# Optimization experiments

Measured on AMD Instinct MI355X. Metric: run time of the kernel, lower is better.

## Reference

```python
import jax, jax.numpy as jnp
import numpy as np

NUM_HEADS = 16
HEAD_DIM = 64
G_CONST = 1.0        # phase='fluid'
CURVATURE = 0.15     # phase='fluid'
EPS = 1e-06


def setup_inputs() -> dict:
    key = jax.random.key(0)
    k1, k2, k3, k4, k5 = jax.random.split(key, 5)
    B, S, D = 4, 4096, 1024
    x = jax.random.normal(k1, (B, S, D), dtype=jnp.float32)
    W_qkv = jax.random.normal(k2, (D, 3 * D), dtype=jnp.float32) * 0.02
    b_qkv = jax.random.normal(k3, (3 * D,), dtype=jnp.float32) * 0.02
    W_out = jax.random.normal(k4, (D, D), dtype=jnp.float32) * 0.02
    b_out = jax.random.normal(k5, (D,), dtype=jnp.float32) * 0.02
    return {"x": x, "W_qkv": W_qkv, "b_qkv": b_qkv, "W_out": W_out, "b_out": b_out}


def reference(x, W_qkv, b_qkv, W_out, b_out):
    B, S, D = x.shape
    H, Hd = NUM_HEADS, HEAD_DIM
    # qkv projection -> (B, S, 3, H, Hd); heads are NOT transposed (faithful to source):
    # attention is computed among the H heads at each token position.
    qkv = (x @ W_qkv + b_qkv).reshape(B, S, 3, H, Hd)
    q, k, v = qkv[:, :, 0], qkv[:, :, 1], qkv[:, :, 2]  # each (B,S,H,Hd)

    # squared euclidean distances between head vectors (matmul-based cdist, clamped >= 0)
    q_sq = jnp.sum(q * q, axis=-1)                      # (B,S,H)
    k_sq = jnp.sum(k * k, axis=-1)                      # (B,S,H)
    qk = jnp.einsum('bshd,bsgd->bshg', q, k)            # (B,S,H,H)
    dist_sq = jnp.maximum(q_sq[..., :, None] + k_sq[..., None, :] - 2.0 * qk, 0.0)

    # curvature cosine modulation (curvature != 0 in 'fluid' phase)
    dist_sq = dist_sq * (1.0 + CURVATURE * jnp.cos(jnp.sqrt(dist_sq + EPS)))

    # gravitational forces: G * m_q m_k / (d^2 + eps)
    m_q = jnp.sqrt(q_sq)                                # (B,S,H)
    m_k = jnp.sqrt(k_sq)                                # (B,S,H)
    forces = G_CONST * (m_q[..., :, None] * m_k[..., None, :]) / (dist_sq + EPS)

    attn = jax.nn.softmax(forces, axis=-1)              # softmax over key-heads
    out = jnp.einsum('bshg,bsgd->bshd', attn, v).reshape(B, S, D)
    return out @ W_out + b_out
```

## Files before the change

kernel.cpp:

```cpp
#include <hip/hip_runtime.h>
#include <hip/hip_bf16.h>
#include <math.h>

#define M_TOTAL 16384
#define D_MODEL 1024
#define N_QKV   3072
#define CURV    0.15f
#define EPS_F   1e-6f

typedef __attribute__((ext_vector_type(8))) short short8v;
typedef __attribute__((ext_vector_type(4))) float f32x4;

__device__ __forceinline__ void gl_lds16(const void* g, void* l) {
    __builtin_amdgcn_global_load_lds(
        (const __attribute__((address_space(1))) void*)g,
        (__attribute__((address_space(3))) void*)l, 16, 0, 0);
}
__device__ __forceinline__ unsigned short f2bf_bits(float x) {
    __hip_bfloat16 t = __float2bfloat16(x);
    return *(unsigned short*)&t;
}
__device__ __forceinline__ float bf2f(unsigned short u) {
    return __uint_as_float(((unsigned)u) << 16);
}

__global__ __launch_bounds__(256)
void cast_f32_bf16(const float* __restrict__ in, unsigned short* __restrict__ out,
                   int ngroups)
{
    int i = blockIdx.x * 256 + threadIdx.x;
    if (i >= ngroups) return;
    float4 u = ((const float4*)in)[i];
    ushort4 r;
    r.x = f2bf_bits(u.x); r.y = f2bf_bits(u.y);
    r.z = f2bf_bits(u.z); r.w = f2bf_bits(u.w);
    ((ushort4*)out)[i] = r;
}

__global__ __launch_bounds__(256)
void transpose_cast(const float* __restrict__ W, unsigned short* __restrict__ Wt,
                    int K, int N)
{
    __shared__ float tile[32][33];
    const int n0 = blockIdx.x * 32;
    const int k0 = blockIdx.y * 32;
    const int tx = threadIdx.x & 31;
    const int ty = threadIdx.x >> 5;
    #pragma unroll
    for (int i = 0; i < 32; i += 8)
        tile[ty + i][tx] = W[(size_t)(k0 + ty + i) * N + n0 + tx];
    __syncthreads();
    #pragma unroll
    for (int i = 0; i < 32; i += 8)
        Wt[(size_t)(n0 + ty + i) * K + k0 + tx] = f2bf_bits(tile[tx][ty + i]);
}

template<int OUT_BF16>
__global__ __launch_bounds__(512, 2)
void gemm256_8ph(const unsigned short* __restrict__ A,
                 const unsigned short* __restrict__ Bt,
                 const float* __restrict__ bias,
                 void* __restrict__ Cout,
                 int M, int N, int K, int nbx)
{
    __shared__ __align__(16) short smem_s[65536];

    const int t    = threadIdx.x;
    const int w    = t >> 6;
    const int lane = t & 63;
    const int wm   = w >> 2;
    const int wn   = w & 3;
    const int lr   = lane & 15;
    const int hi   = lane >> 4;
    const int lo7  = lane & 7;

    const int nwg  = gridDim.x;
    const int orig = blockIdx.x;
    const int wgid = (orig & 7) * (nwg >> 3) + (orig >> 3);
    const int by = wgid / nbx, bx = wgid % nbx;
    const int bm0 = by * 256, bn0 = bx * 256;

    const int nt = K >> 6;

    const int srow = t >> 3;
    const int scol = ((t & 7) ^ (srow & 7)) * 8;
    const unsigned short* Ag = A  + (size_t)(bm0 + srow) * K + scol;
    const unsigned short* Bg = Bt + (size_t)(bn0 + srow) * K + scol;
    const int wbase = w * 1024;

    auto STAGE = [&](int which, int half, int tile) {
        const unsigned short* g0 = (which ? Bg : Ag)
                                 + (size_t)(half * 128) * K + (size_t)tile * 64;
        char* d0 = (char*)smem_s + ((tile & 1) * 65536 + which * 32768
                                    + half * 16384 + wbase);
        gl_lds16(g0,                d0);
        gl_lds16(g0 + (size_t)64*K, d0 + 8192);
    };

    short8v a[8][2], b[4][2];
    f32x4 acc[8][4] = {};

    auto LDA = [&](int buf, int m, int ks) {
        a[m][ks] = *(const short8v*)&smem_s[buf*32768 + wm*8192
                        + (m*16 + lr)*64 + (((ks*4 + hi) ^ lo7) * 8)];
    };
    auto LDB = [&](int buf, int n, int ks) {
        b[n][ks] = *(const short8v*)&smem_s[buf*32768 + 16384 + (wn>>1)*8192
                        + ((wn&1)*64 + n*16 + lr)*64 + (((ks*4 + hi) ^ lo7) * 8)];
    };
    auto QUAD = [&](int mlo, int nlo) {
        __builtin_amdgcn_s_setprio(1);
        #pragma unroll
        for (int mi = 0; mi < 4; ++mi)
            #pragma unroll
            for (int ni = 0; ni < 2; ++ni)
                #pragma unroll
                for (int ks = 0; ks < 2; ++ks)
                    acc[mlo+mi][nlo+ni] = __builtin_amdgcn_mfma_f32_16x16x32_bf16(
                        a[mlo+mi][ks], b[nlo+ni][ks], acc[mlo+mi][nlo+ni], 0, 0, 0);
        __builtin_amdgcn_s_setprio(0);
    };

    STAGE(0,0,0); STAGE(0,1,0); STAGE(1,0,0); STAGE(1,1,0);
    STAGE(0,0,1); STAGE(0,1,1); STAGE(1,0,1); STAGE(1,1,1);
    asm volatile("s_waitcnt vmcnt(8)" ::: "memory");
    __builtin_amdgcn_s_barrier();
    #pragma unroll
    for (int m = 0; m < 4; ++m) { LDA(0,m,0); LDA(0,m,1); }
    LDB(0,0,0); LDB(0,0,1); LDB(0,1,0); LDB(0,1,1);

    for (int T = 0; T < nt; ++T) {
        const int buf  = T & 1;
        const int nbuf = buf ^ 1;
        LDB(buf,2,0); LDB(buf,2,1); LDB(buf,3,0); LDB(buf,3,1);
        asm volatile("s_waitcnt lgkmcnt(4)" ::: "memory");
        __builtin_amdgcn_sched_barrier(0);
        QUAD(0,0);
        #pragma unroll
        for (int m = 4; m < 8; ++m) { LDA(buf,m,0); LDA(buf,m,1); }
        asm volatile("s_waitcnt lgkmcnt(8)" ::: "memory");
        __builtin_amdgcn_sched_barrier(0);
        QUAD(0,2);
        __builtin_amdgcn_s_barrier();
        if (T+2 < nt) { STAGE(1,0,T+2); STAGE(1,1,T+2); }
        asm volatile("s_waitcnt lgkmcnt(0)" ::: "memory");
        __builtin_amdgcn_sched_barrier(0);
        QUAD(4,0);
        __builtin_amdgcn_s_barrier();
        if (T+2 < nt) { STAGE(0,0,T+2); STAGE(0,1,T+2); }
        if (T+2 < nt) { asm volatile("s_waitcnt vmcnt(8)" ::: "memory"); }
        else          { asm volatile("s_waitcnt vmcnt(0)" ::: "memory"); }
        __builtin_amdgcn_s_barrier();
        if (T+1 < nt) {
            #pragma unroll
            for (int m = 0; m < 4; ++m) { LDA(nbuf,m,0); LDA(nbuf,m,1); }
            LDB(nbuf,0,0); LDB(nbuf,0,1); LDB(nbuf,1,0); LDB(nbuf,1,1);
        }
        __builtin_amdgcn_sched_barrier(0);
        QUAD(4,2);
    }

    const int r0 = bm0 + wm*128 + hi*4;
    const int cb = bn0 + wn*64 + lr;
    float bv[4];
    #pragma unroll
    for (int n = 0; n < 4; ++n) bv[n] = bias[cb + n*16];
    if (OUT_BF16) {
        unsigned short* Cb = (unsigned short*)Cout;
        #pragma unroll
        for (int m = 0; m < 8; ++m)
            #pragma unroll
            for (int j = 0; j < 4; ++j) {
                unsigned short* rp = Cb + (size_t)(r0 + m*16 + j) * N;
                #pragma unroll
                for (int n = 0; n < 4; ++n)
                    rp[cb + n*16] = f2bf_bits(acc[m][n][j] + bv[n]);
            }
    } else {
        float* Cf = (float*)Cout;
        #pragma unroll
        for (int m = 0; m < 8; ++m)
            #pragma unroll
            for (int j = 0; j < 4; ++j) {
                float* rp = Cf + (size_t)(r0 + m*16 + j) * N;
                #pragma unroll
                for (int n = 0; n < 4; ++n)
                    rp[cb + n*16] = acc[m][n][j] + bv[n];
            }
    }
}

__global__ __launch_bounds__(256)
void attn_mfma_kernel(const unsigned short* __restrict__ qkv,
                      unsigned short* __restrict__ aout)
{
    const int l  = threadIdx.x & 63;
    const int wv = threadIdx.x >> 6;
    const int p  = blockIdx.x * 4 + wv;
    const int lr = l & 15;
    const int hi = l >> 4;
    const unsigned short* base = qkv + (size_t)p * N_QKV;

    short8v qf0 = *(const short8v*)(base +        lr*64 +      hi*8);
    short8v qf1 = *(const short8v*)(base +        lr*64 + 32 + hi*8);
    short8v kf0 = *(const short8v*)(base + 1024 + lr*64 +      hi*8);
    short8v kf1 = *(const short8v*)(base + 1024 + lr*64 + 32 + hi*8);

    f32x4 s = {};
    s = __builtin_amdgcn_mfma_f32_16x16x32_bf16(kf0, qf0, s, 0, 0, 0);
    s = __builtin_amdgcn_mfma_f32_16x16x32_bf16(kf1, qf1, s, 0, 0, 0);

    float qsq = 0.f, ksq = 0.f;
    #pragma unroll
    for (int i = 0; i < 8; ++i) {
        float q0 = bf2f((unsigned short)qf0[i]), q1 = bf2f((unsigned short)qf1[i]);
        float k0 = bf2f((unsigned short)kf0[i]), k1 = bf2f((unsigned short)kf1[i]);
        qsq = fmaf(q0, q0, fmaf(q1, q1, qsq));
        ksq = fmaf(k0, k0, fmaf(k1, k1, ksq));
    }
    qsq += __shfl_xor(qsq, 16); qsq += __shfl_xor(qsq, 32);
    ksq += __shfl_xor(ksq, 16); ksq += __shfl_xor(ksq, 32);

    const float mq = sqrtf(qsq);

    float P[4];
    #pragma unroll
    for (int j = 0; j < 4; ++j) {
        float ksg = __shfl(ksq, hi * 4 + j);
        float dsq = fmaxf(qsq + ksg - 2.f * s[j], 0.f);
        dsq = dsq * (1.f + CURV * cosf(sqrtf(dsq + EPS_F)));
        P[j] = mq * sqrtf(ksg) / (dsq + EPS_F);
    }
    float mx = fmaxf(fmaxf(P[0], P[1]), fmaxf(P[2], P[3]));
    mx = fmaxf(mx, __shfl_xor(mx, 16));
    mx = fmaxf(mx, __shfl_xor(mx, 32));
    float sm = 0.f;
    #pragma unroll
    for (int j = 0; j < 4; ++j) { P[j] = expf(P[j] - mx); sm += P[j]; }
    sm += __shfl_xor(sm, 16); sm += __shfl_xor(sm, 32);
    const float inv = 1.f / sm;

    unsigned int w0 = (unsigned)f2bf_bits(P[0] * inv)
                    | ((unsigned)f2bf_bits(P[1] * inv) << 16);
    unsigned int w1 = (unsigned)f2bf_bits(P[2] * inv)
                    | ((unsigned)f2bf_bits(P[3] * inv) << 16);
    const int s0 = lr + (((2 * hi)     & 3) << 4);
    const int s1 = lr + (((2 * hi + 1) & 3) << 4);
    unsigned int a0 = __shfl((int)w0, s0), a1 = __shfl((int)w1, s0);
    unsigned int a2 = __shfl((int)w0, s1), a3 = __shfl((int)w1, s1);
    if (hi >= 2) { a0 = a1 = a2 = a3 = 0; }
    unsigned int pa_u[4] = {a0, a1, a2, a3};
    short8v pa = *(short8v*)pa_u;

    const unsigned short* vb = base + 2048;
    unsigned short* orow = aout + (size_t)p * D_MODEL;
    #pragma unroll
    for (int c = 0; c < 4; ++c) {
        unsigned int bu[4];
        #pragma unroll
        for (int e2 = 0; e2 < 4; ++e2) {
            int g0 = (hi * 8 + e2 * 2) & 15;
            int g1 = (hi * 8 + e2 * 2 + 1) & 15;
            unsigned int lo = vb[g0 * 64 + c * 16 + lr];
            unsigned int hi16 = vb[g1 * 64 + c * 16 + lr];
            bu[e2] = lo | (hi16 << 16);
        }
        short8v bv = *(short8v*)bu;
        f32x4 o = {};
        o = __builtin_amdgcn_mfma_f32_16x16x32_bf16(pa, bv, o, 0, 0, 0);
        #pragma unroll
        for (int j = 0; j < 4; ++j)
            orow[(hi * 4 + j) * 64 + c * 16 + lr] = f2bf_bits(o[j]);
    }
}

extern "C" void kernel_launch(void* const* d_in, const int* in_sizes, int n_in,
                              void* d_out, int out_size, void* d_ws, size_t ws_size,
                              hipStream_t stream)
{
    const float* x     = (const float*)d_in[0];
    const float* W_qkv = (const float*)d_in[1];
    const float* b_qkv = (const float*)d_in[2];
    const float* W_out = (const float*)d_in[3];
    const float* b_out = (const float*)d_in[4];
    float* out = (float*)d_out;

    char* ws = (char*)d_ws;
    unsigned short* qkvb = (unsigned short*)ws;
    unsigned short* xb   = (unsigned short*)(ws + (size_t)M_TOTAL * N_QKV * 2);
    unsigned short* ab   = xb;
    unsigned short* Wt1  = (unsigned short*)(ws + (size_t)M_TOTAL * N_QKV * 2
                                                + (size_t)M_TOTAL * D_MODEL * 2);
    unsigned short* Wt2  = Wt1 + (size_t)N_QKV * D_MODEL;

    {
        int ngroups = M_TOTAL * D_MODEL / 4;
        cast_f32_bf16<<<ngroups / 256, 256, 0, stream>>>(x, xb, ngroups);
    }
    {
        dim3 g(N_QKV / 32, D_MODEL / 32);
        transpose_cast<<<g, 256, 0, stream>>>(W_qkv, Wt1, D_MODEL, N_QKV);
        dim3 g2(D_MODEL / 32, D_MODEL / 32);
        transpose_cast<<<g2, 256, 0, stream>>>(W_out, Wt2, D_MODEL, D_MODEL);
    }

    {
        int nbx = N_QKV / 256;
        int nwg = (M_TOTAL / 256) * nbx;
        gemm256_8ph<1><<<nwg, 512, 0, stream>>>(xb, Wt1, b_qkv, qkvb,
                                                M_TOTAL, N_QKV, D_MODEL, nbx);
    }

    attn_mfma_kernel<<<M_TOTAL / 4, 256, 0, stream>>>(qkvb, ab);

    {
        int nbx = D_MODEL / 256;
        int nwg = (M_TOTAL / 256) * nbx;
        gemm256_8ph<0><<<nwg, 512, 0, stream>>>(ab, Wt2, b_out, out,
                                                M_TOTAL, D_MODEL, D_MODEL, nbx);
    }
}
```

Measured before the change: 191.4 us.

## Replace eight-phase interleaved GEMM main loop with single-phase load-then-compute schedule

The GEMM main loop no longer interleaves LDS fragment reads with MFMA quadrants and staggered global-to-LDS stages. Each k-tile now loads all A and B fragments up front, runs every MFMA in one block, and then issues all four stages for tile T+2 between two barriers. This simplifies the schedule and may cut barrier and waitcnt overhead. It gives up overlap of LDS reads with MFMA work and lets the compiler pick the order of memory waits.

```diff
diff --git a/kernel.cpp b/kernel.cpp
--- a/kernel.cpp
+++ b/kernel.cpp
@@ -57,7 +57,7 @@
 
 template<int OUT_BF16>
 __global__ __launch_bounds__(512, 2)
-void gemm256_8ph(const unsigned short* __restrict__ A,
+void gemm256_1ph(const unsigned short* __restrict__ A,
                  const unsigned short* __restrict__ Bt,
                  const float* __restrict__ bias,
                  void* __restrict__ Cout,
@@ -108,56 +108,44 @@
         b[n][ks] = *(const short8v*)&smem_s[buf*32768 + 16384 + (wn>>1)*8192
                         + ((wn&1)*64 + n*16 + lr)*64 + (((ks*4 + hi) ^ lo7) * 8)];
     };
-    auto QUAD = [&](int mlo, int nlo) {
-        __builtin_amdgcn_s_setprio(1);
-        #pragma unroll
-        for (int mi = 0; mi < 4; ++mi)
-            #pragma unroll
-            for (int ni = 0; ni < 2; ++ni)
-                #pragma unroll
-                for (int ks = 0; ks < 2; ++ks)
-                    acc[mlo+mi][nlo+ni] = __builtin_amdgcn_mfma_f32_16x16x32_bf16(
-                        a[mlo+mi][ks], b[nlo+ni][ks], acc[mlo+mi][nlo+ni], 0, 0, 0);
-        __builtin_amdgcn_s_setprio(0);
-    };
 
     STAGE(0,0,0); STAGE(0,1,0); STAGE(1,0,0); STAGE(1,1,0);
     STAGE(0,0,1); STAGE(0,1,1); STAGE(1,0,1); STAGE(1,1,1);
     asm volatile("s_waitcnt vmcnt(8)" ::: "memory");
     __builtin_amdgcn_s_barrier();
-    #pragma unroll
-    for (int m = 0; m < 4; ++m) { LDA(0,m,0); LDA(0,m,1); }
-    LDB(0,0,0); LDB(0,0,1); LDB(0,1,0); LDB(0,1,1);
-
-    for (int T = 0; T < nt; ++T) {
-        const int buf  = T & 1;
-        const int nbuf = buf ^ 1;
-        LDB(buf,2,0); LDB(buf,2,1); LDB(buf,3,0); LDB(buf,3,1);
-        asm volatile("s_waitcnt lgkmcnt(4)" ::: "memory");
-        __builtin_amdgcn_sched_barrier(0);
-        QUAD(0,0);
-        #pragma unroll
-        for (int m = 4; m < 8; ++m) { LDA(buf,m,0); LDA(buf,m,1); }
-        asm volatile("s_waitcnt lgkmcnt(8)" ::: "memory");
-        __builtin_amdgcn_sched_barrier(0);
-        QUAD(0,2);
-        __builtin_amdgcn_s_barrier();
-        if (T+2 < nt) { STAGE(1,0,T+2); STAGE(1,1,T+2); }
-        asm volatile("s_waitcnt lgkmcnt(0)" ::: "memory");
-        __builtin_amdgcn_sched_barrier(0);
-        QUAD(4,0);
-        __builtin_amdgcn_s_barrier();
-        if (T+2 < nt) { STAGE(0,0,T+2); STAGE(0,1,T+2); }
-        if (T+2 < nt) { asm volatile("s_waitcnt vmcnt(8)" ::: "memory"); }
-        else          { asm volatile("s_waitcnt vmcnt(0)" ::: "memory"); }
-        __builtin_amdgcn_s_barrier();
-        if (T+1 < nt) {
-            #pragma unroll
-            for (int m = 0; m < 4; ++m) { LDA(nbuf,m,0); LDA(nbuf,m,1); }
-            LDB(nbuf,0,0); LDB(nbuf,0,1); LDB(nbuf,1,0); LDB(nbuf,1,1);
+
+    for (int T2 = 0; T2 < nt; T2 += 2) {
+        #pragma unroll
+        for (int u = 0; u < 2; ++u) {
+            const int T = T2 + u;
+            #pragma unroll
+            for (int m = 0; m < 8; ++m) LDA(u, m, 0);
+            #pragma unroll
+            for (int n = 0; n < 4; ++n) LDB(u, n, 0);
+            #pragma unroll
+            for (int m = 0; m < 8; ++m) LDA(u, m, 1);
+            #pragma unroll
+            for (int n = 0; n < 4; ++n) LDB(u, n, 1);
+            __builtin_amdgcn_s_setprio(1);
+            #pragma unroll
+            for (int ks = 0; ks < 2; ++ks)
+                #pragma unroll
+                for (int n = 0; n < 4; ++n)
+                    #pragma unroll
+                    for (int m = 0; m < 8; ++m)
+                        acc[m][n] = __builtin_amdgcn_mfma_f32_16x16x32_bf16(
+                                        a[m][ks], b[n][ks], acc[m][n], 0, 0, 0);
+            __builtin_amdgcn_s_setprio(0);
+            __builtin_amdgcn_s_barrier();
+            if (T + 2 < nt) {
+                STAGE(0,0,T+2); STAGE(0,1,T+2);
+                STAGE(1,0,T+2); STAGE(1,1,T+2);
+                asm volatile("s_waitcnt vmcnt(8)" ::: "memory");
+            } else {
+                asm volatile("s_waitcnt vmcnt(0)" ::: "memory");
+            }
+            __builtin_amdgcn_s_barrier();
         }
-        __builtin_amdgcn_sched_barrier(0);
-        QUAD(4,2);
     }
 
     const int r0 = bm0 + wm*128 + hi*4;
@@ -307,7 +295,7 @@
     {
         int nbx = N_QKV / 256;
         int nwg = (M_TOTAL / 256) * nbx;
-        gemm256_8ph<1><<<nwg, 512, 0, stream>>>(xb, Wt1, b_qkv, qkvb,
+        gemm256_1ph<1><<<nwg, 512, 0, stream>>>(xb, Wt1, b_qkv, qkvb,
                                                 M_TOTAL, N_QKV, D_MODEL, nbx);
     }
 
@@ -316,7 +304,7 @@
     {
         int nbx = D_MODEL / 256;
         int nwg = (M_TOTAL / 256) * nbx;
-        gemm256_8ph<0><<<nwg, 512, 0, stream>>>(ab, Wt2, b_out, out,
+        gemm256_1ph<0><<<nwg, 512, 0, stream>>>(ab, Wt2, b_out, out,
                                                 M_TOTAL, D_MODEL, D_MODEL, nbx);
     }
 }
```

New measurement: 218.5 us. 1.14x slower.
